# Kernel optimization log

Measured on AMD Instinct MI355X. Metric: run time of the kernel, lower is better.

Reference implementation:

```python
import jax, jax.numpy as jnp
import numpy as np

B, T, H, PRED = 16384, 8, 256, 12


def _cell(x, h, c, Wih, Whh, bih, bhh):
    # PyTorch LSTM gate order: i, f, g, o
    g = x @ Wih.T + h @ Whh.T + bih + bhh
    i, f, gg, o = jnp.split(g, 4, axis=-1)
    c = jax.nn.sigmoid(f) * c + jax.nn.sigmoid(i) * jnp.tanh(gg)
    h = jax.nn.sigmoid(o) * jnp.tanh(c)
    return h, c


def _run_seq(x, layers):
    # stacked LSTM over full sequence, zero initial state; x: [B, T, D]
    b = x.shape[0]
    inp = x
    hs, cs = [], []
    for (Wih, Whh, bih, bhh) in layers:
        h0 = jnp.zeros((b, Whh.shape[1]), x.dtype)

        def step(carry, xt, Wih=Wih, Whh=Whh, bih=bih, bhh=bhh):
            h, c = _cell(xt, carry[0], carry[1], Wih, Whh, bih, bhh)
            return (h, c), h

        (h, c), out = jax.lax.scan(step, (h0, h0), jnp.swapaxes(inp, 0, 1))
        inp = jnp.swapaxes(out, 0, 1)
        hs.append(h)
        cs.append(c)
    return inp, jnp.stack(hs), jnp.stack(cs)


def _step_stack(x, hs, cs, layers):
    # single-timestep pass through stacked LSTM; hs/cs: [L, B, H]
    inp = x
    nh, nc = [], []
    for l, (Wih, Whh, bih, bhh) in enumerate(layers):
        h, c = _cell(inp, hs[l], cs[l], Wih, Whh, bih, bhh)
        inp = h
        nh.append(h)
        nc.append(c)
    return inp, jnp.stack(nh), jnp.stack(nc)


def _forward(x, l1_Wih0, l1_Whh0, l1_bih0, l1_bhh0, l1_Wih1, l1_Whh1, l1_bih1, l1_bhh1,
             l2_Wih0, l2_Whh0, l2_bih0, l2_bhh0, l2_Wih1, l2_Whh1, l2_bih1, l2_bhh1,
             fc1_w, fc1_b, fc2_w, fc2_b):
    L1 = [(l1_Wih0, l1_Whh0, l1_bih0, l1_bhh0), (l1_Wih1, l1_Whh1, l1_bih1, l1_bhh1)]
    L2 = [(l2_Wih0, l2_Whh0, l2_bih0, l2_bhh0), (l2_Wih1, l2_Whh1, l2_bih1, l2_bhh1)]
    out1, h1, c1 = _run_seq(x, L1)           # encode observed track
    _, h2, c2 = _run_seq(out1, L2)
    pos = x[:, -1, :]

    def dec(carry, _):
        pos, h1, c1, h2, c2 = carry
        o1, h1, c1 = _step_stack(pos, h1, c1, L1)
        o2, h2, c2 = _step_stack(o1, h2, c2, L2)
        delta = jax.nn.relu(o2 @ fc1_w.T + fc1_b) @ fc2_w.T + fc2_b
        pos = pos + delta
        return (pos, h1, c1, h2, c2), pos

    _, preds = jax.lax.scan(dec, (pos, h1, c1, h2, c2), None, length=PRED)
    return jnp.swapaxes(preds, 0, 1)  # [B, PRED, 2]


def setup_inputs() -> dict:
    key = jax.random.key(0)
    ks = iter(jax.random.split(key, 32))
    s = 1.0 / np.sqrt(H)  # matches PyTorch LSTM/Linear init scale

    def mk(shape):
        return jax.random.uniform(next(ks), shape, jnp.float32, -s, s)

    d = {"x": jax.random.normal(next(ks), (B, T, 2), jnp.float32)}
    for name, in_dim in [("l1", 2), ("l2", H)]:
        for layer in range(2):
            di = in_dim if layer == 0 else H
            d[f"{name}_Wih{layer}"] = mk((4 * H, di))
            d[f"{name}_Whh{layer}"] = mk((4 * H, H))
            d[f"{name}_bih{layer}"] = mk((4 * H,))
            d[f"{name}_bhh{layer}"] = mk((4 * H,))
    d["fc1_w"] = mk((H, H))
    d["fc1_b"] = mk((H,))
    d["fc2_w"] = mk((2, H))
    d["fc2_b"] = mk((2,))
    return d


def reference(x, l1_Wih0, l1_Whh0, l1_bih0, l1_bhh0, l1_Wih1, l1_Whh1, l1_bih1, l1_bhh1,
              l2_Wih0, l2_Whh0, l2_bih0, l2_bhh0, l2_Wih1, l2_Whh1, l2_bih1, l2_bhh1,
              fc1_w, fc1_b, fc2_w, fc2_b):
    return _forward(x, l1_Wih0, l1_Whh0, l1_bih0, l1_bhh0, l1_Wih1, l1_Whh1, l1_bih1, l1_bhh1,
                    l2_Wih0, l2_Whh0, l2_bih0, l2_bhh0, l2_Wih1, l2_Whh1, l2_bih1, l2_bhh1,
                    fc1_w, fc1_b, fc2_w, fc2_b)
```

## Files before the change

kernel.cpp:

```cpp
#include <hip/hip_runtime.h>
#include <stdint.h>

#define Bsz   16384
#define Tseq  8
#define NPRED 12

typedef __attribute__((ext_vector_type(4))) float    f32x4;
typedef _Float16 h16;
typedef __attribute__((ext_vector_type(8))) _Float16 h16x8;

__device__ __forceinline__ float sigf(float x)   { return 1.f / (1.f + __expf(-x)); }
__device__ __forceinline__ float tanh_f(float x) { return 1.f - 2.f / (__expf(2.f * x) + 1.f); }

__device__ __forceinline__ void gload_lds16(const void* g, void* l) {
  __builtin_amdgcn_global_load_lds(
      (const __attribute__((address_space(1))) void*)g,
      (__attribute__((address_space(3))) void*)l, 16, 0, 0);
}

__global__ void zero_r7(f32x4* __restrict__ p, long n4) {
  long i = (long)blockIdx.x * 256 + threadIdx.x;
  f32x4 z; z[0] = 0.f; z[1] = 0.f; z[2] = 0.f; z[3] = 0.f;
  if (i < n4) p[i] = z;
}
__global__ void mark_r7(float* __restrict__ out) {
  if (blockIdx.x == 0 && threadIdx.x < 64) out[threadIdx.x] = 1000.0f;
}
__global__ void seed_r7(float* __restrict__ pos, const float* __restrict__ x) {
  int b = blockIdx.x * 256 + threadIdx.x;
  pos[2 * b]     = x[(size_t)b * 16 + 14];
  pos[2 * b + 1] = x[(size_t)b * 16 + 15];
}

__global__ void pack_w(h16* __restrict__ dst, const float* __restrict__ W0,
                       const float* __restrict__ W1, int ksplit, int Kw, int Np,
                       int gatePack) {
  int idx = blockIdx.x * 256 + threadIdx.x;
  if (idx >= Np * Kw) return;
  int np = idx / Kw, k = idx - np * Kw;
  int n = np;
  if (gatePack) { int jb = np >> 7, gi = (np >> 5) & 3, jr = np & 31; n = gi * 256 + jb * 32 + jr; }
  float w = (k < ksplit) ? W0[(size_t)n * ksplit + k]
                         : W1[(size_t)n * (Kw - ksplit) + (k - ksplit)];
  uint32_t byte = (uint32_t)np * (uint32_t)(Kw * 2) + (((uint32_t)k * 2) ^ (uint32_t)((np & 7) << 4));
  *(h16*)((char*)dst + byte) = (h16)w;
}

__global__ void add_bias(float* __restrict__ dst, const float* __restrict__ a,
                         const float* __restrict__ b) {
  int i = blockIdx.x * 256 + threadIdx.x;
  if (i < 1024) dst[i] = a[i] + b[i];
}

template <int NSEG, int HASX, int LSTM>
__global__ __launch_bounds__(256) void cell_gemm(
    const char* __restrict__ A0, const char* __restrict__ A1,
    const char* __restrict__ Wp, int Kw, int NY,
    const float* __restrict__ bias, const float* __restrict__ wih0,
    const float* __restrict__ xbase, int xstride,
    float* __restrict__ Cst, char* __restrict__ hout) {
  __shared__ __align__(16) char lds[32768];
  char* ldsA = lds;
  char* ldsB = lds + 16384;
  const int tid = threadIdx.x;
  const int wave = tid >> 6, lane = tid & 63;

  int lid = blockIdx.x;
  int chunkv = gridDim.x >> 3;
  int swz = (lid & 7) * chunkv + (lid >> 3);
  const int by = swz % NY, bx = swz / NY;
  const int m0 = bx * 128;
  const int n0 = by * 128;

  f32x4 acc[2][8];
#pragma unroll
  for (int m = 0; m < 2; m++)
#pragma unroll
    for (int n = 0; n < 8; n++)
#pragma unroll
      for (int e = 0; e < 4; e++) acc[m][n][e] = 0.f;

  const int rowa = tid >> 3;
  const int chb  = (tid & 7) * 16;
  const int KB   = Kw >> 6;

  for (int kb = 0; kb < KB; ++kb) {
    const char* Asrc; int k0;
    if (NSEG == 2 && kb >= 4) { Asrc = A1; k0 = (kb - 4) << 6; }
    else                      { Asrc = A0; k0 = kb << 6; }
#pragma unroll
    for (int it = 0; it < 4; ++it) {
      gload_lds16(Asrc + (size_t)(m0 + it * 32 + rowa) * 512 + k0 * 2 + chb,
                  ldsA + it * 4096 + wave * 1024);
      gload_lds16(Wp + (size_t)(n0 + it * 32 + rowa) * (Kw * 2) + kb * 128 + chb,
                  ldsB + it * 4096 + wave * 1024);
    }
    __syncthreads();
#pragma unroll
    for (int kk = 0; kk < 2; ++kk) {
      const int kbyte = kk * 64 + (lane >> 4) * 16;
      h16x8 af[2], bfr[8];
#pragma unroll
      for (int mt = 0; mt < 2; ++mt) {
        int r = wave * 32 + mt * 16 + (lane & 15);
        af[mt] = *(const h16x8*)(ldsA + r * 128 + (kbyte ^ ((r & 7) << 4)));
      }
#pragma unroll
      for (int nt = 0; nt < 8; ++nt) {
        int cc = nt * 16 + (lane & 15);
        bfr[nt] = *(const h16x8*)(ldsB + cc * 128 + (kbyte ^ ((cc & 7) << 4)));
      }
#pragma unroll
      for (int mt = 0; mt < 2; ++mt)
#pragma unroll
        for (int nt = 0; nt < 8; ++nt)
          acc[mt][nt] = __builtin_amdgcn_mfma_f32_16x16x32_f16(af[mt], bfr[nt], acc[mt][nt], 0, 0, 0);
    }
    __syncthreads();
  }

  if constexpr (LSTM) {
#pragma unroll
    for (int c = 0; c < 2; c++) {
      const int j = (n0 >> 2) + c * 16 + (lane & 15);
      const float bi = bias[j], bff = bias[256 + j], bg = bias[512 + j], bo = bias[768 + j];
      float wi0 = 0, wi1 = 0, wf0 = 0, wf1 = 0, wg0 = 0, wg1 = 0, wo0 = 0, wo1 = 0;
      if constexpr (HASX) {
        wi0 = wih0[2 * j];           wi1 = wih0[2 * j + 1];
        wf0 = wih0[2 * (256 + j)];   wf1 = wih0[2 * (256 + j) + 1];
        wg0 = wih0[2 * (512 + j)];   wg1 = wih0[2 * (512 + j) + 1];
        wo0 = wih0[2 * (768 + j)];   wo1 = wih0[2 * (768 + j) + 1];
      }
#pragma unroll
      for (int mt = 0; mt < 2; ++mt) {
#pragma unroll
        for (int e = 0; e < 4; e++) {
          const int b = m0 + wave * 32 + mt * 16 + (lane >> 4) * 4 + e;
          float vi = acc[mt][0 + c][e] + bi;
          float vf = acc[mt][2 + c][e] + bff;
          float vg = acc[mt][4 + c][e] + bg;
          float vo = acc[mt][6 + c][e] + bo;
          if constexpr (HASX) {
            const float x0 = xbase[(size_t)b * xstride];
            const float x1 = xbase[(size_t)b * xstride + 1];
            vi += x0 * wi0 + x1 * wi1;
            vf += x0 * wf0 + x1 * wf1;
            vg += x0 * wg0 + x1 * wg1;
            vo += x0 * wo0 + x1 * wo1;
          }
          const size_t ci = (size_t)b * 256 + j;
          float cn = sigf(vf) * Cst[ci] + sigf(vi) * tanh_f(vg);
          float h  = sigf(vo) * tanh_f(cn);
          Cst[ci] = cn;
          *(h16*)(hout + (size_t)b * 512 + (((unsigned)j * 2) ^ (unsigned)((b & 7) << 4))) = (h16)h;
        }
      }
    }
  } else {
#pragma unroll
    for (int nt = 0; nt < 8; ++nt) {
      const int n = n0 + nt * 16 + (lane & 15);
      const float bn = bias[n];
#pragma unroll
      for (int mt = 0; mt < 2; ++mt)
#pragma unroll
        for (int e = 0; e < 4; e++) {
          const int b = m0 + wave * 32 + mt * 16 + (lane >> 4) * 4 + e;
          float v = acc[mt][nt][e] + bn;
          v = v > 0.f ? v : 0.f;
          *(h16*)(hout + (size_t)b * 512 + (((unsigned)n * 2) ^ (unsigned)((b & 7) << 4))) = (h16)v;
        }
    }
  }
}

__global__ void fc2_pos(const char* __restrict__ r, const float* __restrict__ w,
                        const float* __restrict__ fb, float* __restrict__ pos,
                        float* __restrict__ out, int s) {
  int b = blockIdx.x * 256 + threadIdx.x;
  float a0 = fb[0], a1 = fb[1];
#pragma unroll
  for (int ch = 0; ch < 32; ch++) {
    h16x8 v = *(const h16x8*)(r + (size_t)b * 512 + (((unsigned)ch * 16) ^ (unsigned)((b & 7) << 4)));
#pragma unroll
    for (int e = 0; e < 8; e++) {
      float rv = (float)v[e];
      int k = ch * 8 + e;
      a0 += rv * w[k];
      a1 += rv * w[256 + k];
    }
  }
  float p0 = pos[2 * b] + a0;
  float p1 = pos[2 * b + 1] + a1;
  pos[2 * b] = p0;
  pos[2 * b + 1] = p1;
  out[(size_t)b * (NPRED * 2) + s * 2]     = p0;
  out[(size_t)b * (NPRED * 2) + s * 2 + 1] = p1;
}

extern "C" void kernel_launch(void* const* d_in, const int* in_sizes, int n_in,
                              void* d_out, int out_size, void* d_ws, size_t ws_size,
                              hipStream_t stream) {
  const float* x      = (const float*)d_in[0];
  const float* Wih[4] = {(const float*)d_in[1], (const float*)d_in[5],
                         (const float*)d_in[9], (const float*)d_in[13]};
  const float* Whh[4] = {(const float*)d_in[2], (const float*)d_in[6],
                         (const float*)d_in[10], (const float*)d_in[14]};
  const float* bih[4] = {(const float*)d_in[3], (const float*)d_in[7],
                         (const float*)d_in[11], (const float*)d_in[15]};
  const float* bhh[4] = {(const float*)d_in[4], (const float*)d_in[8],
                         (const float*)d_in[12], (const float*)d_in[16]};
  const float* fc1_w = (const float*)d_in[17];
  const float* fc1_b = (const float*)d_in[18];
  const float* fc2_w = (const float*)d_in[19];
  const float* fc2_b = (const float*)d_in[20];

  char* ws = (char*)d_ws;
  size_t off = 0;
  auto alloc = [&](size_t bytes) -> char* {
    char* p = ws + off;
    off += (bytes + 255) & ~(size_t)255;
    return p;
  };

  float* Cs[4];
  for (int l = 0; l < 4; l++) Cs[l] = (float*)alloc((size_t)Bsz * 256 * 4);
  char* zeroh = alloc((size_t)Bsz * 512);
  char* h10[2] = {alloc((size_t)Bsz * 512), alloc((size_t)Bsz * 512)};
  char* sl[2]  = {alloc((size_t)Bsz * 512), alloc((size_t)Bsz * 512)};
  char* h20[2] = {alloc((size_t)Bsz * 512), alloc((size_t)Bsz * 512)};
  char* h21[2] = {alloc((size_t)Bsz * 512), alloc((size_t)Bsz * 512)};
  char* rbuf = alloc((size_t)Bsz * 512);
  float* pos = (float*)alloc((size_t)Bsz * 2 * 4);
  float* biasc = (float*)alloc(4 * 1024 * 4);
  h16* wp10 = (h16*)alloc((size_t)1024 * 256 * 2);
  h16* wp[3];
  for (int i = 0; i < 3; i++) wp[i] = (h16*)alloc((size_t)1024 * 512 * 2);
  h16* wpf1 = (h16*)alloc((size_t)256 * 256 * 2);

  if (ws_size < off) {
    mark_r7<<<dim3(1), dim3(64), 0, stream>>>((float*)d_out);
    return;
  }

  {
    long n4 = ((size_t)Bsz * 256 * 4 * 4 + (size_t)Bsz * 512) / 16;
    zero_r7<<<dim3((unsigned)((n4 + 255) / 256)), dim3(256), 0, stream>>>((f32x4*)Cs[0], n4);
  }
  seed_r7<<<dim3(Bsz / 256), dim3(256), 0, stream>>>(pos, x);

  pack_w<<<dim3((1024 * 256 + 255) / 256), dim3(256), 0, stream>>>(wp10, Whh[0], Whh[0], 256, 256, 1024, 1);
  pack_w<<<dim3((1024 * 512 + 255) / 256), dim3(256), 0, stream>>>(wp[0], Wih[1], Whh[1], 256, 512, 1024, 1);
  pack_w<<<dim3((1024 * 512 + 255) / 256), dim3(256), 0, stream>>>(wp[1], Wih[2], Whh[2], 256, 512, 1024, 1);
  pack_w<<<dim3((1024 * 512 + 255) / 256), dim3(256), 0, stream>>>(wp[2], Wih[3], Whh[3], 256, 512, 1024, 1);
  pack_w<<<dim3((256 * 256 + 255) / 256), dim3(256), 0, stream>>>(wpf1, fc1_w, fc1_w, 256, 256, 256, 0);
  for (int l = 0; l < 4; l++)
    add_bias<<<dim3(4), dim3(256), 0, stream>>>(biasc + l * 1024, bih[l], bhh[l]);

  for (int t = 0; t < Tseq; t++) {
    int cur = t & 1, prev = cur ^ 1;
    const char* h10r = (t == 0) ? zeroh : h10[prev];
    const char* slr  = (t == 0) ? zeroh : sl[prev];
    const char* h20r = (t == 0) ? zeroh : h20[prev];
    const char* h21r = (t == 0) ? zeroh : h21[prev];
    cell_gemm<1, 1, 1><<<dim3(1024), dim3(256), 0, stream>>>(
        h10r, zeroh, (const char*)wp10, 256, 8, biasc, Wih[0], x + t * 2, 16, Cs[0], h10[cur]);
    cell_gemm<2, 0, 1><<<dim3(1024), dim3(256), 0, stream>>>(
        h10[cur], slr, (const char*)wp[0], 512, 8, biasc + 1024, nullptr, nullptr, 0, Cs[1], sl[cur]);
    cell_gemm<2, 0, 1><<<dim3(1024), dim3(256), 0, stream>>>(
        sl[cur], h20r, (const char*)wp[1], 512, 8, biasc + 2048, nullptr, nullptr, 0, Cs[2], h20[cur]);
    cell_gemm<2, 0, 1><<<dim3(1024), dim3(256), 0, stream>>>(
        h20[cur], h21r, (const char*)wp[2], 512, 8, biasc + 3072, nullptr, nullptr, 0, Cs[3], h21[cur]);
  }

  for (int s = 0; s < NPRED; s++) {
    int u = Tseq + s, cur = u & 1, prev = cur ^ 1;
    cell_gemm<1, 1, 1><<<dim3(1024), dim3(256), 0, stream>>>(
        h10[prev], zeroh, (const char*)wp10, 256, 8, biasc, Wih[0], pos, 2, Cs[0], h10[cur]);
    cell_gemm<2, 0, 1><<<dim3(1024), dim3(256), 0, stream>>>(
        h10[cur], sl[prev], (const char*)wp[0], 512, 8, biasc + 1024, nullptr, nullptr, 0, Cs[1], sl[cur]);
    cell_gemm<2, 0, 1><<<dim3(1024), dim3(256), 0, stream>>>(
        sl[cur], h20[prev], (const char*)wp[1], 512, 8, biasc + 2048, nullptr, nullptr, 0, Cs[2], h20[cur]);
    cell_gemm<2, 0, 1><<<dim3(1024), dim3(256), 0, stream>>>(
        h20[cur], h21[prev], (const char*)wp[2], 512, 8, biasc + 3072, nullptr, nullptr, 0, Cs[3], h21[cur]);
    cell_gemm<1, 0, 0><<<dim3(256), dim3(256), 0, stream>>>(
        h21[cur], zeroh, (const char*)wpf1, 256, 2, fc1_b, nullptr, nullptr, 0, nullptr, rbuf);
    fc2_pos<<<dim3(Bsz / 256), dim3(256), 0, stream>>>(rbuf, fc2_w, fc2_b, pos, (float*)d_out, s);
  }
}
```

Before: 2.788 ms.

## Wavefront-schedule encoder LSTM cells diagonally and retile GEMM to 2x2 wave layout

Runs the encoder as a diagonal wavefront: each launch computes all (layer, timestep) cells whose inputs are ready, so up to four independent cell GEMMs share one grid instead of four serial launches per step. The GEMM core is also retiled so the four waves cover a 2x2 grid of 64x64 subtiles. Packed weights move to a kb-blocked contiguous layout so each K-block tile is one contiguous 16KB chunk. A launch-bounds occupancy hint of 4 blocks is added. The intent is fewer launches and dependency bubbles and better per-wave fragment reuse, at the cost of extra register pressure and a runtime-indexed descriptor struct.

Result: faster. 2.393 ms (-14.2%).

```diff
diff --git a/kernel.cpp b/kernel.cpp
--- a/kernel.cpp
+++ b/kernel.cpp
@@ -18,15 +18,15 @@
       (__attribute__((address_space(3))) void*)l, 16, 0, 0);
 }
 
-__global__ void zero_r7(f32x4* __restrict__ p, long n4) {
+__global__ void zero_r10(f32x4* __restrict__ p, long n4) {
   long i = (long)blockIdx.x * 256 + threadIdx.x;
   f32x4 z; z[0] = 0.f; z[1] = 0.f; z[2] = 0.f; z[3] = 0.f;
   if (i < n4) p[i] = z;
 }
-__global__ void mark_r7(float* __restrict__ out) {
+__global__ void mark_r10(float* __restrict__ out) {
   if (blockIdx.x == 0 && threadIdx.x < 64) out[threadIdx.x] = 1000.0f;
 }
-__global__ void seed_r7(float* __restrict__ pos, const float* __restrict__ x) {
+__global__ void seed_r10(float* __restrict__ pos, const float* __restrict__ x) {
   int b = blockIdx.x * 256 + threadIdx.x;
   pos[2 * b]     = x[(size_t)b * 16 + 14];
   pos[2 * b + 1] = x[(size_t)b * 16 + 15];
@@ -39,10 +39,16 @@
   if (idx >= Np * Kw) return;
   int np = idx / Kw, k = idx - np * Kw;
   int n = np;
-  if (gatePack) { int jb = np >> 7, gi = (np >> 5) & 3, jr = np & 31; n = gi * 256 + jb * 32 + jr; }
+  if (gatePack) {
+    int jb = np >> 7, wc = (np >> 6) & 1, gi = (np >> 4) & 3, jr = np & 15;
+    n = gi * 256 + jb * 32 + wc * 16 + jr;
+  }
   float w = (k < ksplit) ? W0[(size_t)n * ksplit + k]
                          : W1[(size_t)n * (Kw - ksplit) + (k - ksplit)];
-  uint32_t byte = (uint32_t)np * (uint32_t)(Kw * 2) + (((uint32_t)k * 2) ^ (uint32_t)((np & 7) << 4));
+  int KB = Kw >> 6;
+  int jb = np >> 7, r = np & 127, kb = k >> 6;
+  uint32_t byte = (uint32_t)(jb * KB + kb) * 16384u + (uint32_t)r * 128u
+                + ((2u * (uint32_t)(k & 63)) ^ (uint32_t)((r & 7) << 4));
   *(h16*)((char*)dst + byte) = (h16)w;
 }
 
@@ -52,120 +58,160 @@
   if (i < 1024) dst[i] = a[i] + b[i];
 }
 
+__device__ __forceinline__ void gemm_core(
+    const char* A0, const char* A1, const char* Wp, int KB, int by, int m0,
+    char* ldsA, char* ldsB, int tid, f32x4 acc[4][4]) {
+  const int wave = tid >> 6, lane = tid & 63;
+  const int rowa = tid >> 3;
+  const int chb  = (tid & 7) * 16;
+
+#pragma unroll
+  for (int m = 0; m < 4; m++)
+#pragma unroll
+    for (int n = 0; n < 4; n++)
+#pragma unroll
+      for (int e = 0; e < 4; e++) acc[m][n][e] = 0.f;
+
+  const char* aCur   = A0 + (size_t)(m0 + rowa) * 512 + chb;
+  const char* a1Base = A1 + (size_t)(m0 + rowa) * 512 + chb;
+  const char* wCur   = Wp + (size_t)by * KB * 16384 + rowa * 128 + chb;
+
+  const int wr = wave >> 1, wc = wave & 1;
+
+  for (int kb = 0; kb < KB; ++kb) {
+    if (kb == 4) aCur = a1Base;
+#pragma unroll
+    for (int it = 0; it < 4; ++it) {
+      gload_lds16(aCur + it * 16384, ldsA + it * 4096 + wave * 1024);
+      gload_lds16(wCur + it * 4096,  ldsB + it * 4096 + wave * 1024);
+    }
+    __syncthreads();
+#pragma unroll
+    for (int kk = 0; kk < 2; ++kk) {
+      const int kbyte = kk * 64 + (lane >> 4) * 16;
+      h16x8 af[4], bfr[4];
+#pragma unroll
+      for (int mt = 0; mt < 4; ++mt) {
+        int r = wr * 64 + mt * 16 + (lane & 15);
+        af[mt] = *(const h16x8*)(ldsA + r * 128 + (kbyte ^ ((r & 7) << 4)));
+      }
+#pragma unroll
+      for (int nt = 0; nt < 4; ++nt) {
+        int c = wc * 64 + nt * 16 + (lane & 15);
+        bfr[nt] = *(const h16x8*)(ldsB + c * 128 + (kbyte ^ ((c & 7) << 4)));
+      }
+#pragma unroll
+      for (int mt = 0; mt < 4; ++mt)
+#pragma unroll
+        for (int nt = 0; nt < 4; ++nt)
+          acc[mt][nt] = __builtin_amdgcn_mfma_f32_16x16x32_f16(af[mt], bfr[nt], acc[mt][nt], 0, 0, 0);
+    }
+    __syncthreads();
+    aCur += 128;
+    wCur += 16384;
+  }
+}
+
+__device__ __forceinline__ void lstm_epilogue(
+    f32x4 acc[4][4], int m0, int n0, int tid, const float* bias,
+    const float* wih0, const float* xbase, int xstride, int hasx,
+    float* Cst, char* hout) {
+  const int wave = tid >> 6, lane = tid & 63;
+  const int wr = wave >> 1, wc = wave & 1;
+  const int j = (n0 >> 2) + wc * 16 + (lane & 15);
+  const float bi = bias[j], bff = bias[256 + j], bg = bias[512 + j], bo = bias[768 + j];
+  float wi0 = 0, wi1 = 0, wf0 = 0, wf1 = 0, wg0 = 0, wg1 = 0, wo0 = 0, wo1 = 0;
+  if (hasx) {
+    wi0 = wih0[2 * j];           wi1 = wih0[2 * j + 1];
+    wf0 = wih0[2 * (256 + j)];   wf1 = wih0[2 * (256 + j) + 1];
+    wg0 = wih0[2 * (512 + j)];   wg1 = wih0[2 * (512 + j) + 1];
+    wo0 = wih0[2 * (768 + j)];   wo1 = wih0[2 * (768 + j) + 1];
+  }
+#pragma unroll
+  for (int mt = 0; mt < 4; ++mt) {
+#pragma unroll
+    for (int e = 0; e < 4; e++) {
+      const int b = m0 + wr * 64 + mt * 16 + (lane >> 4) * 4 + e;
+      float vi = acc[mt][0][e] + bi;
+      float vf = acc[mt][1][e] + bff;
+      float vg = acc[mt][2][e] + bg;
+      float vo = acc[mt][3][e] + bo;
+      if (hasx) {
+        const float x0 = xbase[(size_t)b * xstride];
+        const float x1 = xbase[(size_t)b * xstride + 1];
+        vi += x0 * wi0 + x1 * wi1;
+        vf += x0 * wf0 + x1 * wf1;
+        vg += x0 * wg0 + x1 * wg1;
+        vo += x0 * wo0 + x1 * wo1;
+      }
+      const size_t ci = (size_t)b * 256 + j;
+      float cn = sigf(vf) * Cst[ci] + sigf(vi) * tanh_f(vg);
+      float h  = sigf(vo) * tanh_f(cn);
+      Cst[ci] = cn;
+      *(h16*)(hout + (size_t)b * 512 + (((unsigned)j * 2) ^ (unsigned)((b & 7) << 4))) = (h16)h;
+    }
+  }
+}
+
+struct CellDesc {
+  const char* A0; const char* A1; const char* Wp;
+  const float* bias; const float* wih0; const float* xbase;
+  float* Cst; char* hout;
+  int Kw; int xstride; int hasx;
+};
+struct Fused4 { CellDesc c[4]; };
+
+__global__ __launch_bounds__(256, 4) void cells_diag(Fused4 args) {
+  const int cellid = blockIdx.x >> 10;
+  const int lid    = blockIdx.x & 1023;
+  const CellDesc d = args.c[cellid];
+
+  __shared__ __align__(16) char lds[32768];
+  const int tid = threadIdx.x;
+
+  int swz = (lid & 7) * 128 + (lid >> 3);
+  const int by = swz & 7, bx = swz >> 3;
+  const int m0 = bx * 128, n0 = by * 128;
+
+  f32x4 acc[4][4];
+  gemm_core(d.A0, d.A1, d.Wp, d.Kw >> 6, by, m0, lds, lds + 16384, tid, acc);
+  lstm_epilogue(acc, m0, n0, tid, d.bias, d.wih0, d.xbase, d.xstride, d.hasx,
+                d.Cst, d.hout);
+}
+
 template <int NSEG, int HASX, int LSTM>
-__global__ __launch_bounds__(256) void cell_gemm(
+__global__ __launch_bounds__(256, 4) void cell_gemm(
     const char* __restrict__ A0, const char* __restrict__ A1,
     const char* __restrict__ Wp, int Kw, int NY,
     const float* __restrict__ bias, const float* __restrict__ wih0,
     const float* __restrict__ xbase, int xstride,
     float* __restrict__ Cst, char* __restrict__ hout) {
   __shared__ __align__(16) char lds[32768];
-  char* ldsA = lds;
-  char* ldsB = lds + 16384;
   const int tid = threadIdx.x;
-  const int wave = tid >> 6, lane = tid & 63;
 
   int lid = blockIdx.x;
   int chunkv = gridDim.x >> 3;
   int swz = (lid & 7) * chunkv + (lid >> 3);
   const int by = swz % NY, bx = swz / NY;
-  const int m0 = bx * 128;
-  const int n0 = by * 128;
-
-  f32x4 acc[2][8];
-#pragma unroll
-  for (int m = 0; m < 2; m++)
-#pragma unroll
-    for (int n = 0; n < 8; n++)
-#pragma unroll
-      for (int e = 0; e < 4; e++) acc[m][n][e] = 0.f;
-
-  const int rowa = tid >> 3;
-  const int chb  = (tid & 7) * 16;
-  const int KB   = Kw >> 6;
-
-  for (int kb = 0; kb < KB; ++kb) {
-    const char* Asrc; int k0;
-    if (NSEG == 2 && kb >= 4) { Asrc = A1; k0 = (kb - 4) << 6; }
-    else                      { Asrc = A0; k0 = kb << 6; }
-#pragma unroll
-    for (int it = 0; it < 4; ++it) {
-      gload_lds16(Asrc + (size_t)(m0 + it * 32 + rowa) * 512 + k0 * 2 + chb,
-                  ldsA + it * 4096 + wave * 1024);
-      gload_lds16(Wp + (size_t)(n0 + it * 32 + rowa) * (Kw * 2) + kb * 128 + chb,
-                  ldsB + it * 4096 + wave * 1024);
-    }
-    __syncthreads();
-#pragma unroll
-    for (int kk = 0; kk < 2; ++kk) {
-      const int kbyte = kk * 64 + (lane >> 4) * 16;
-      h16x8 af[2], bfr[8];
-#pragma unroll
-      for (int mt = 0; mt < 2; ++mt) {
-        int r = wave * 32 + mt * 16 + (lane & 15);
-        af[mt] = *(const h16x8*)(ldsA + r * 128 + (kbyte ^ ((r & 7) << 4)));
-      }
-#pragma unroll
-      for (int nt = 0; nt < 8; ++nt) {
-        int cc = nt * 16 + (lane & 15);
-        bfr[nt] = *(const h16x8*)(ldsB + cc * 128 + (kbyte ^ ((cc & 7) << 4)));
-      }
-#pragma unroll
-      for (int mt = 0; mt < 2; ++mt)
-#pragma unroll
-        for (int nt = 0; nt < 8; ++nt)
-          acc[mt][nt] = __builtin_amdgcn_mfma_f32_16x16x32_f16(af[mt], bfr[nt], acc[mt][nt], 0, 0, 0);
-    }
-    __syncthreads();
-  }
+  const int m0 = bx * 128, n0 = by * 128;
+
+  f32x4 acc[4][4];
+  gemm_core(A0, NSEG == 2 ? A1 : A0, Wp, Kw >> 6, by, m0, lds, lds + 16384, tid, acc);
 
   if constexpr (LSTM) {
-#pragma unroll
-    for (int c = 0; c < 2; c++) {
-      const int j = (n0 >> 2) + c * 16 + (lane & 15);
-      const float bi = bias[j], bff = bias[256 + j], bg = bias[512 + j], bo = bias[768 + j];
-      float wi0 = 0, wi1 = 0, wf0 = 0, wf1 = 0, wg0 = 0, wg1 = 0, wo0 = 0, wo1 = 0;
-      if constexpr (HASX) {
-        wi0 = wih0[2 * j];           wi1 = wih0[2 * j + 1];
-        wf0 = wih0[2 * (256 + j)];   wf1 = wih0[2 * (256 + j) + 1];
-        wg0 = wih0[2 * (512 + j)];   wg1 = wih0[2 * (512 + j) + 1];
-        wo0 = wih0[2 * (768 + j)];   wo1 = wih0[2 * (768 + j) + 1];
-      }
-#pragma unroll
-      for (int mt = 0; mt < 2; ++mt) {
+    lstm_epilogue(acc, m0, n0, tid, bias, wih0, xbase, xstride, HASX, Cst, hout);
+  } else {
+    const int wave = tid >> 6, lane = tid & 63;
+    const int wr = wave >> 1, wc = wave & 1;
+#pragma unroll
+    for (int nt = 0; nt < 4; ++nt) {
+      const int n = n0 + wc * 64 + nt * 16 + (lane & 15);
+      const float bn = bias[n];
+#pragma unroll
+      for (int mt = 0; mt < 4; ++mt)
 #pragma unroll
         for (int e = 0; e < 4; e++) {
-          const int b = m0 + wave * 32 + mt * 16 + (lane >> 4) * 4 + e;
-          float vi = acc[mt][0 + c][e] + bi;
-          float vf = acc[mt][2 + c][e] + bff;
-          float vg = acc[mt][4 + c][e] + bg;
-          float vo = acc[mt][6 + c][e] + bo;
-          if constexpr (HASX) {
-            const float x0 = xbase[(size_t)b * xstride];
-            const float x1 = xbase[(size_t)b * xstride + 1];
-            vi += x0 * wi0 + x1 * wi1;
-            vf += x0 * wf0 + x1 * wf1;
-            vg += x0 * wg0 + x1 * wg1;
-            vo += x0 * wo0 + x1 * wo1;
-          }
-          const size_t ci = (size_t)b * 256 + j;
-          float cn = sigf(vf) * Cst[ci] + sigf(vi) * tanh_f(vg);
-          float h  = sigf(vo) * tanh_f(cn);
-          Cst[ci] = cn;
-          *(h16*)(hout + (size_t)b * 512 + (((unsigned)j * 2) ^ (unsigned)((b & 7) << 4))) = (h16)h;
-        }
-      }
-    }
-  } else {
-#pragma unroll
-    for (int nt = 0; nt < 8; ++nt) {
-      const int n = n0 + nt * 16 + (lane & 15);
-      const float bn = bias[n];
-#pragma unroll
-      for (int mt = 0; mt < 2; ++mt)
-#pragma unroll
-        for (int e = 0; e < 4; e++) {
-          const int b = m0 + wave * 32 + mt * 16 + (lane >> 4) * 4 + e;
+          const int b = m0 + wr * 64 + mt * 16 + (lane >> 4) * 4 + e;
           float v = acc[mt][nt][e] + bn;
           v = v > 0.f ? v : 0.f;
           *(h16*)(hout + (size_t)b * 512 + (((unsigned)n * 2) ^ (unsigned)((b & 7) << 4))) = (h16)v;
@@ -239,15 +285,15 @@
   h16* wpf1 = (h16*)alloc((size_t)256 * 256 * 2);
 
   if (ws_size < off) {
-    mark_r7<<<dim3(1), dim3(64), 0, stream>>>((float*)d_out);
+    mark_r10<<<dim3(1), dim3(64), 0, stream>>>((float*)d_out);
     return;
   }
 
   {
     long n4 = ((size_t)Bsz * 256 * 4 * 4 + (size_t)Bsz * 512) / 16;
-    zero_r7<<<dim3((unsigned)((n4 + 255) / 256)), dim3(256), 0, stream>>>((f32x4*)Cs[0], n4);
-  }
-  seed_r7<<<dim3(Bsz / 256), dim3(256), 0, stream>>>(pos, x);
+    zero_r10<<<dim3((unsigned)((n4 + 255) / 256)), dim3(256), 0, stream>>>((f32x4*)Cs[0], n4);
+  }
+  seed_r10<<<dim3(Bsz / 256), dim3(256), 0, stream>>>(pos, x);
 
   pack_w<<<dim3((1024 * 256 + 255) / 256), dim3(256), 0, stream>>>(wp10, Whh[0], Whh[0], 256, 256, 1024, 1);
   pack_w<<<dim3((1024 * 512 + 255) / 256), dim3(256), 0, stream>>>(wp[0], Wih[1], Whh[1], 256, 512, 1024, 1);
@@ -257,20 +303,30 @@
   for (int l = 0; l < 4; l++)
     add_bias<<<dim3(4), dim3(256), 0, stream>>>(biasc + l * 1024, bih[l], bhh[l]);
 
-  for (int t = 0; t < Tseq; t++) {
-    int cur = t & 1, prev = cur ^ 1;
-    const char* h10r = (t == 0) ? zeroh : h10[prev];
-    const char* slr  = (t == 0) ? zeroh : sl[prev];
-    const char* h20r = (t == 0) ? zeroh : h20[prev];
-    const char* h21r = (t == 0) ? zeroh : h21[prev];
-    cell_gemm<1, 1, 1><<<dim3(1024), dim3(256), 0, stream>>>(
-        h10r, zeroh, (const char*)wp10, 256, 8, biasc, Wih[0], x + t * 2, 16, Cs[0], h10[cur]);
-    cell_gemm<2, 0, 1><<<dim3(1024), dim3(256), 0, stream>>>(
-        h10[cur], slr, (const char*)wp[0], 512, 8, biasc + 1024, nullptr, nullptr, 0, Cs[1], sl[cur]);
-    cell_gemm<2, 0, 1><<<dim3(1024), dim3(256), 0, stream>>>(
-        sl[cur], h20r, (const char*)wp[1], 512, 8, biasc + 2048, nullptr, nullptr, 0, Cs[2], h20[cur]);
-    cell_gemm<2, 0, 1><<<dim3(1024), dim3(256), 0, stream>>>(
-        h20[cur], h21r, (const char*)wp[2], 512, 8, biasc + 3072, nullptr, nullptr, 0, Cs[3], h21[cur]);
+  char* hbuf[4][2] = {{h10[0], h10[1]}, {sl[0], sl[1]}, {h20[0], h20[1]}, {h21[0], h21[1]}};
+  const h16* wpl[4] = {wp10, wp[0], wp[1], wp[2]};
+  for (int d = 0; d <= 10; d++) {
+    Fused4 args;
+    int nc = 0;
+    for (int l = 0; l < 4; l++) {
+      int t = d - l;
+      if (t < 0 || t >= Tseq) continue;
+      CellDesc& cd = args.c[nc++];
+      cd.A0 = (l == 0) ? ((t == 0) ? zeroh : hbuf[0][(t - 1) & 1])
+                       : hbuf[l - 1][t & 1];
+      cd.A1 = (l == 0) ? zeroh
+                       : ((t == 0) ? zeroh : hbuf[l][(t - 1) & 1]);
+      cd.Wp = (const char*)wpl[l];
+      cd.bias = biasc + l * 1024;
+      cd.wih0 = (l == 0) ? Wih[0] : nullptr;
+      cd.xbase = (l == 0) ? (x + t * 2) : nullptr;
+      cd.Cst = Cs[l];
+      cd.hout = hbuf[l][t & 1];
+      cd.Kw = (l == 0) ? 256 : 512;
+      cd.xstride = 16;
+      cd.hasx = (l == 0) ? 1 : 0;
+    }
+    cells_diag<<<dim3(nc * 1024), dim3(256), 0, stream>>>(args);
   }
 
   for (int s = 0; s < NPRED; s++) {
```
